# Kernel tuning notes

Measured on AMD Instinct MI355X. Metric: run time of the kernel, lower is better.

The kernel has to match this reference:

```python
import jax, jax.numpy as jnp
import numpy as np

D_MODEL, N_HEAD, D_HEAD = 192, 12, 16
S, B, RLEN = 1024, 4, 2048
LN_EPS = 1e-12


def _xavier(key, shape):
    fan_in, fan_out = shape[0], int(np.prod(shape[1:]))
    limit = float(np.sqrt(6.0 / (fan_in + fan_out)))
    return jax.random.uniform(key, shape, jnp.float32, -limit, limit)


def setup_inputs() -> dict:
    key = jax.random.key(0)
    ks = jax.random.split(key, 12)
    inp = {
        "x": jax.random.normal(ks[0], (S, B, D_MODEL), jnp.float32),
        "r": jax.random.normal(ks[1], (RLEN, B, D_MODEL), jnp.float32),
        "mask0": jnp.zeros((S, S, B, 1), jnp.float32),
        "Wq": _xavier(ks[2], (D_MODEL, N_HEAD, D_HEAD)),
        "Wk": _xavier(ks[3], (D_MODEL, N_HEAD, D_HEAD)),
        "Wv": _xavier(ks[4], (D_MODEL, N_HEAD, D_HEAD)),
        "Wo": _xavier(ks[5], (D_MODEL, N_HEAD, D_HEAD)),
        "Wr": _xavier(ks[6], (D_MODEL, N_HEAD, D_HEAD)),
        "r_w_bias": _xavier(ks[7], (N_HEAD, D_HEAD)),
        "r_r_bias": _xavier(ks[8], (N_HEAD, D_HEAD)),
        "ln_w": jnp.ones((D_MODEL,), jnp.float32),
        "ln_b": jnp.zeros((D_MODEL,), jnp.float32),
    }
    return inp


def _rel_shift_bnij(x, klen):
    # x: [b, n, i, j] with j = rlen; XLNet relative shift, keep first klen cols
    b, n, i, j = x.shape
    x = x.reshape(b, n, j, i)[:, :, 1:, :].reshape(b, n, i, j - 1)
    return x[:, :, :, :klen]


def reference(x, r, mask0, Wq, Wk, Wv, Wo, Wr, r_w_bias, r_r_bias, ln_w, ln_b):
    mask0 = jnp.zeros_like(mask0)  # Model.forward zeroes the mask
    q_head = jnp.einsum("ibh,hnd->ibnd", x, Wq)
    k_head = jnp.einsum("ibh,hnd->ibnd", x, Wk)
    v_head = jnp.einsum("ibh,hnd->ibnd", x, Wv)
    k_head_r = jnp.einsum("ibh,hnd->ibnd", r, Wr)

    # content-based score
    ac = jnp.einsum("ibnd,jbnd->bnij", q_head + r_w_bias, k_head)
    # position-based score with relative shift
    bd = jnp.einsum("ibnd,jbnd->bnij", q_head + r_r_bias, k_head_r)
    bd = _rel_shift_bnij(bd, ac.shape[3])
    # seg_mat is None -> segment term ef = 0

    scale = 1.0 / np.sqrt(D_HEAD)
    attn_score = (ac + bd) * scale
    attn_score = attn_score - 1e30 * jnp.einsum("ijbn->bnij", mask0)
    attn_prob = jax.nn.softmax(attn_score, axis=3)

    attn_vec = jnp.einsum("bnij,jbnd->ibnd", attn_prob, v_head)
    attn_out = jnp.einsum("ibnd,hnd->ibh", attn_vec, Wo)

    out = attn_out + x  # residual
    mean = jnp.mean(out, axis=-1, keepdims=True)
    var = jnp.mean(jnp.square(out - mean), axis=-1, keepdims=True)
    out = (out - mean) * jax.lax.rsqrt(var + LN_EPS) * ln_w + ln_b
    return out
```

## Files before the change

kernel.cpp:

```cpp
#include <hip/hip_runtime.h>
#include <hip/hip_bf16.h>

#define SQ   1024
#define BB   4
#define DM   192
#define NH   12
#define DH   16
#define RL   2048
#define BN   (BB*NH)

typedef __attribute__((ext_vector_type(8))) short  short8;
typedef __attribute__((ext_vector_type(4))) float  f32x4;
typedef __attribute__((ext_vector_type(2))) unsigned u32x2;
typedef __attribute__((ext_vector_type(4))) unsigned u32x4;

__device__ __forceinline__ short f2bf(float f) {
    unsigned u = __float_as_uint(f);
    u += 0x7fff + ((u >> 16) & 1);
    return (short)(u >> 16);
}
__device__ __forceinline__ unsigned pkbf(float lo, float hi) {
    union { __hip_bfloat162 h; unsigned u; } cv;
    cv.h = __float22bfloat162_rn(make_float2(lo, hi));
    return cv.u;
}
#define P32SWAP(a, b) asm volatile("v_permlane32_swap_b32 %0, %1" : "+v"(a), "+v"(b))
#define P16SWAP(a, b) asm volatile("v_permlane16_swap_b32 %0, %1" : "+v"(a), "+v"(b))

__global__ __launch_bounds__(256) void k_prep(
    const float* __restrict__ x, const float* __restrict__ r,
    const float* __restrict__ Wq, const float* __restrict__ Wk,
    const float* __restrict__ Wv, const float* __restrict__ Wr,
    const float* __restrict__ Wo,
    unsigned short* __restrict__ xb, unsigned short* __restrict__ rb,
    unsigned short* __restrict__ WTq, unsigned short* __restrict__ WTk,
    unsigned short* __restrict__ WTv, unsigned short* __restrict__ WTr,
    unsigned short* __restrict__ Wob)
{
    int idx = blockIdx.x * 256 + threadIdx.x;
    if (idx < 786432) { xb[idx] = (unsigned short)f2bf(x[idx]); return; }
    idx -= 786432;
    if (idx < 1572864) { rb[idx] = (unsigned short)f2bf(r[idx]); return; }
    idx -= 1572864;
    if (idx < 36864) { int nd = idx / 192, h = idx % 192;
                       WTq[idx] = (unsigned short)f2bf(Wq[h*192 + nd]); return; }
    idx -= 36864;
    if (idx < 36864) { int nd = idx / 192, h = idx % 192;
                       WTk[idx] = (unsigned short)f2bf(Wk[h*192 + nd]); return; }
    idx -= 36864;
    if (idx < 36864) { int nd = idx / 192, h = idx % 192;
                       WTv[idx] = (unsigned short)f2bf(Wv[h*192 + nd]); return; }
    idx -= 36864;
    if (idx < 36864) { int nd = idx / 192, h = idx % 192;
                       WTr[idx] = (unsigned short)f2bf(Wr[h*192 + nd]); return; }
    idx -= 36864;
    if (idx < 36864) { Wob[idx] = (unsigned short)f2bf(Wo[idx]); return; }
}

__global__ __launch_bounds__(256) void k_gemm_xr(
    const unsigned short* __restrict__ xb, const unsigned short* __restrict__ rbm,
    const unsigned short* __restrict__ WTq, const unsigned short* __restrict__ WTk,
    const unsigned short* __restrict__ WTv, const unsigned short* __restrict__ WTr,
    const float* __restrict__ rwb, const float* __restrict__ rrb,
    unsigned short* __restrict__ qwb, unsigned short* __restrict__ qrb,
    unsigned short* __restrict__ kh, unsigned short* __restrict__ vh,
    unsigned short* __restrict__ kr)
{
    int bid = blockIdx.x;
    int tid = threadIdx.x, w = tid >> 6, lane = tid & 63, g = lane >> 4, mm = lane & 15;
    if (bid < 2304) {
        int rt = bid / 9, ch = bid % 9;
        int wsel = ch / 3, sub = ch % 3;
        int c0 = sub * 64 + w * 16;
        const unsigned short* WT = (wsel == 0) ? WTq : ((wsel == 1) ? WTk : WTv);
        const unsigned short* arow = xb + (size_t)(rt*16 + mm) * 192 + 8*g;
        const unsigned short* brow = WT + (size_t)(c0 + mm) * 192 + 8*g;
        f32x4 acc = {0.f, 0.f, 0.f, 0.f};
        #pragma unroll
        for (int kk = 0; kk < 6; ++kk) {
            short8 a = *(const short8*)(arow + kk*32);
            short8 b = *(const short8*)(brow + kk*32);
            acc = __builtin_amdgcn_mfma_f32_16x16x32_bf16(a, b, acc, 0, 0, 0);
        }
        int col = c0 + mm, n = col >> 4, d = col & 15;
        if (wsel == 0) {
            const float SCL = 0.3606737602222409f;
            float bw = rwb[col], br = rrb[col];
            #pragma unroll
            for (int r = 0; r < 4; ++r) {
                int row = rt*16 + 4*g + r;
                int i = row >> 2, b2 = row & 3;
                size_t o = ((size_t)(b2*NH + n) * SQ + i) * DH + d;
                qwb[o] = (unsigned short)f2bf((acc[r] + bw) * SCL);
                qrb[o] = (unsigned short)f2bf((acc[r] + br) * SCL);
            }
        } else {
            unsigned short* dst = (wsel == 1) ? kh : vh;
            #pragma unroll
            for (int r = 0; r < 4; ++r) {
                int row = rt*16 + 4*g + r;
                int i = row >> 2, b2 = row & 3;
                size_t o = ((size_t)(b2*NH + n) * SQ + i) * DH + d;
                dst[o] = (unsigned short)f2bf(acc[r]);
            }
        }
    } else {
        int bb = bid - 2304;
        int rt = bb / 3, sub = bb % 3;
        int c0 = sub * 64 + w * 16;
        const unsigned short* arow = rbm + (size_t)(rt*16 + mm) * 192 + 8*g;
        const unsigned short* brow = WTr + (size_t)(c0 + mm) * 192 + 8*g;
        f32x4 acc = {0.f, 0.f, 0.f, 0.f};
        #pragma unroll
        for (int kk = 0; kk < 6; ++kk) {
            short8 a = *(const short8*)(arow + kk*32);
            short8 b = *(const short8*)(brow + kk*32);
            acc = __builtin_amdgcn_mfma_f32_16x16x32_bf16(a, b, acc, 0, 0, 0);
        }
        int col = c0 + mm, n = col >> 4, d = col & 15;
        #pragma unroll
        for (int r = 0; r < 4; ++r) {
            int row = rt*16 + 4*g + r;
            int j = row >> 2, b2 = row & 3;
            kr[((size_t)(b2*NH + n) * RL + j) * DH + d] = (unsigned short)f2bf(acc[r]);
        }
    }
}

__global__ __launch_bounds__(256, 3) void k_attn_mfma(
    const unsigned short* __restrict__ qwb, const unsigned short* __restrict__ qrb,
    const unsigned short* __restrict__ kh, const unsigned short* __restrict__ vh,
    const unsigned short* __restrict__ kr, unsigned short* __restrict__ av_b)
{
    __shared__ __align__(16) short kbuf[2][64*16];
    __shared__ __align__(16) short vbuf[2][64*16];
    __shared__ __align__(16) short rbuf[256*16];
    __shared__ __align__(16) float bdls[4][80*20];

    int bid = blockIdx.x;
    int logical = (bid & 7) * 96 + (bid >> 3);
    int bn = logical >> 4;
    int i0b = (logical & 15) * 64;
    int tid = threadIdx.x, w = tid >> 6, lane = tid & 63;
    int g = lane >> 4, mm = lane & 15;
    size_t headK = (size_t)bn * SQ * DH;
    size_t headR = (size_t)bn * RL * DH;

    short8 qwf = {0,0,0,0,0,0,0,0}, qrf = {0,0,0,0,0,0,0,0};
    if (g < 2) {
        int qrow = i0b + 16*w + mm;
        qwf = *(const short8*)((const short*)qwb + headK + (size_t)qrow*DH + 8*g);
        qrf = *(const short8*)((const short*)qrb + headK + (size_t)qrow*DH + 8*g);
    }

    {
        int hh = tid & 1;
        if (tid < 128) {
            int rr2 = tid >> 1;
            *(u32x4*)(&kbuf[0][rr2*16 + hh*8]) =
                *(const u32x4*)(kh + headK + (size_t)rr2*16 + hh*8);
        } else {
            int rr2 = (tid - 128) >> 1;
            *(u32x4*)(&vbuf[0][rr2*16 + hh*8]) =
                *(const u32x4*)(vh + headK + (size_t)rr2*16 + hh*8);
        }
        int rr2 = tid >> 1;
        int m = 960 - i0b + rr2;
        *(u32x4*)(&rbuf[(m & 255)*16 + hh*8]) =
            *(const u32x4*)(kr + headR + (size_t)m*16 + hh*8);
    }
    __syncthreads();

    float Lacc = 0.f;
    f32x4 opv = {0.f,0.f,0.f,0.f};
    float* bw_ = &bdls[w][0];
    const int basew0 = 1008 - i0b - 16*w;
    const f32x4 z = {0.f,0.f,0.f,0.f};

    for (int t = 0; t < 16; ++t) {
        int cur = t & 1;
        u32x4 sa = {0,0,0,0}, sb = {0,0,0,0};
        bool ds = (t < 15);
        if (ds) {
            if (w == 0) {
                const unsigned short* p = kh + headK + (size_t)(64*(t+1) + lane)*16;
                sa = *(const u32x4*)p; sb = *(const u32x4*)(p + 8);
            } else if (w == 1) {
                const unsigned short* p = vh + headK + (size_t)(64*(t+1) + lane)*16;
                sa = *(const u32x4*)p; sb = *(const u32x4*)(p + 8);
            } else if (w == 2) {
                int m = 1088 + 64*t - i0b + lane;
                const unsigned short* p = kr + headR + (size_t)m*16;
                sa = *(const u32x4*)p; sb = *(const u32x4*)(p + 8);
            }
        }

        int mb = basew0 + 64*t;
        #pragma unroll
        for (int tau = 0; tau < 5; ++tau) {
            int mr = (mb + 16*tau + mm) & 255;
            short8 ra = *(const short8*)(rbuf + mr*16 + 8*(g & 1));
            f32x4 bd = __builtin_amdgcn_mfma_f32_16x16x32_bf16(ra, qrf, z, 0, 0, 0);
            #pragma unroll
            for (int r = 0; r < 4; ++r)
                bw_[(16*tau + 4*g + r)*20 + mm] = bd[r];
        }

        unsigned pk[8]; float Lc = 0.f;
        #pragma unroll
        for (int tp = 0; tp < 4; ++tp) {
            short8 ka = *(const short8*)(&kbuf[cur][(16*tp + mm)*16 + 8*(g & 1)]);
            f32x4 ac = __builtin_amdgcn_mfma_f32_16x16x32_bf16(ka, qwf, z, 0, 0, 0);
            float p0 = __builtin_amdgcn_exp2f(ac[0] + bw_[(16*tp + 4*g + 0 + 16 - mm)*20 + mm]);
            float p1 = __builtin_amdgcn_exp2f(ac[1] + bw_[(16*tp + 4*g + 1 + 16 - mm)*20 + mm]);
            float p2 = __builtin_amdgcn_exp2f(ac[2] + bw_[(16*tp + 4*g + 2 + 16 - mm)*20 + mm]);
            float p3 = __builtin_amdgcn_exp2f(ac[3] + bw_[(16*tp + 4*g + 3 + 16 - mm)*20 + mm]);
            Lc += (p0 + p1) + (p2 + p3);
            pk[2*tp]     = pkbf(p0, p1);
            pk[2*tp + 1] = pkbf(p2, p3);
        }
        Lacc += Lc;

        P32SWAP(pk[0], pk[2]); P16SWAP(pk[0], pk[2]);
        P32SWAP(pk[1], pk[3]); P16SWAP(pk[1], pk[3]);
        P32SWAP(pk[4], pk[6]); P16SWAP(pk[4], pk[6]);
        P32SWAP(pk[5], pk[7]); P16SWAP(pk[5], pk[7]);

        unsigned vb0 = (unsigned)(size_t)(&vbuf[cur][0])
                     + ((unsigned)mm << 3) + ((unsigned)g << 8);
        {
            u32x2 t0, t1;
            asm volatile("ds_read_b64_tr_b16 %0, %2 offset:0\n\t"
                         "ds_read_b64_tr_b16 %1, %2 offset:128\n\t"
                         "s_waitcnt lgkmcnt(0)"
                         : "=&v"(t0), "=&v"(t1) : "v"(vb0));
            __builtin_amdgcn_sched_barrier(0);
            union { unsigned u[4]; short8 s; } va, pb;
            va.u[0]=t0[0]; va.u[1]=t0[1]; va.u[2]=t1[0]; va.u[3]=t1[1];
            pb.u[0]=pk[0]; pb.u[1]=pk[1]; pb.u[2]=pk[2]; pb.u[3]=pk[3];
            opv = __builtin_amdgcn_mfma_f32_16x16x32_bf16(va.s, pb.s, opv, 0, 0, 0);
        }
        {
            u32x2 t0, t1;
            asm volatile("ds_read_b64_tr_b16 %0, %2 offset:0\n\t"
                         "ds_read_b64_tr_b16 %1, %2 offset:128\n\t"
                         "s_waitcnt lgkmcnt(0)"
                         : "=&v"(t0), "=&v"(t1) : "v"(vb0 + 1024));
            __builtin_amdgcn_sched_barrier(0);
            union { unsigned u[4]; short8 s; } va, pb;
            va.u[0]=t0[0]; va.u[1]=t0[1]; va.u[2]=t1[0]; va.u[3]=t1[1];
            pb.u[0]=pk[4]; pb.u[1]=pk[5]; pb.u[2]=pk[6]; pb.u[3]=pk[7];
            opv = __builtin_amdgcn_mfma_f32_16x16x32_bf16(va.s, pb.s, opv, 0, 0, 0);
        }

        if (ds) {
            if (w == 0) {
                *(u32x4*)(&kbuf[cur^1][lane*16])     = sa;
                *(u32x4*)(&kbuf[cur^1][lane*16 + 8]) = sb;
            } else if (w == 1) {
                *(u32x4*)(&vbuf[cur^1][lane*16])     = sa;
                *(u32x4*)(&vbuf[cur^1][lane*16 + 8]) = sb;
            } else if (w == 2) {
                int ms = (1088 + 64*t - i0b + lane) & 255;
                *(u32x4*)(&rbuf[ms*16])     = sa;
                *(u32x4*)(&rbuf[ms*16 + 8]) = sb;
            }
        }
        __syncthreads();
    }

    Lacc += __shfl_xor(Lacc, 16);
    Lacc += __shfl_xor(Lacc, 32);
    float inv = 1.0f / Lacc;
    int b2 = bn / NH, nn = bn % NH;
    int i = i0b + 16*w + mm;
    unsigned o0 = pkbf(opv[0]*inv, opv[1]*inv);
    unsigned o1 = pkbf(opv[2]*inv, opv[3]*inv);
    u32x2 ov = {o0, o1};
    *(u32x2*)(av_b + ((size_t)i*4 + b2)*192 + nn*16 + 4*g) = ov;
}

__global__ __launch_bounds__(256) void k_out_ln(
    const unsigned short* __restrict__ avb, const unsigned short* __restrict__ Wob,
    const float* __restrict__ x,
    const float* __restrict__ lnw, const float* __restrict__ lnb,
    float* __restrict__ out)
{
    __shared__ __align__(16) float os[16][196];
    int tid = threadIdx.x, w = tid >> 6, lane = tid & 63, g = lane >> 4, mm = lane & 15;
    int rt = blockIdx.x;
    const unsigned short* arow = avb + (size_t)(rt*16 + mm)*192 + 8*g;
    short8 a[6];
    #pragma unroll
    for (int kk = 0; kk < 6; ++kk) a[kk] = *(const short8*)(arow + kk*32);
    #pragma unroll
    for (int s = 0; s < 3; ++s) {
        int c0 = w*48 + s*16;
        const unsigned short* brow = Wob + (size_t)(c0 + mm)*192 + 8*g;
        f32x4 acc = {0.f,0.f,0.f,0.f};
        #pragma unroll
        for (int kk = 0; kk < 6; ++kk) {
            short8 b = *(const short8*)(brow + kk*32);
            acc = __builtin_amdgcn_mfma_f32_16x16x32_bf16(a[kk], b, acc, 0, 0, 0);
        }
        int col = c0 + mm;
        #pragma unroll
        for (int r = 0; r < 4; ++r) {
            int rl = 4*g + r;
            os[rl][col] = acc[r] + x[(size_t)(rt*16 + rl)*192 + col];
        }
    }
    __syncthreads();
    int row = tid >> 4, seg = tid & 15;
    const float* ors = &os[row][0] + seg*12;
    f32x4 v0 = *(const f32x4*)(ors);
    f32x4 v1 = *(const f32x4*)(ors + 4);
    f32x4 v2 = *(const f32x4*)(ors + 8);
    float s1 = ((v0[0]+v0[1])+(v0[2]+v0[3])) + ((v1[0]+v1[1])+(v1[2]+v1[3]))
             + ((v2[0]+v2[1])+(v2[2]+v2[3]));
    float q1 = ((v0[0]*v0[0]+v0[1]*v0[1])+(v0[2]*v0[2]+v0[3]*v0[3]))
             + ((v1[0]*v1[0]+v1[1]*v1[1])+(v1[2]*v1[2]+v1[3]*v1[3]))
             + ((v2[0]*v2[0]+v2[1]*v2[1])+(v2[2]*v2[2]+v2[3]*v2[3]));
    #pragma unroll
    for (int off = 1; off < 16; off <<= 1) {
        s1 += __shfl_xor(s1, off);
        q1 += __shfl_xor(q1, off);
    }
    float mean = s1 * (1.0f / 192.0f);
    float var  = q1 * (1.0f / 192.0f) - mean * mean;
    float rstd = rsqrtf(var + 1e-12f);
    int c0 = seg * 12;
    size_t ro = (size_t)(rt*16 + row) * 192;
    #pragma unroll
    for (int c = 0; c < 12; ++c) {
        float v = (c < 4) ? v0[c] : ((c < 8) ? v1[c-4] : v2[c-8]);
        out[ro + c0 + c] = (v - mean) * rstd * lnw[c0 + c] + lnb[c0 + c];
    }
}

extern "C" void kernel_launch(void* const* d_in, const int* in_sizes, int n_in,
                              void* d_out, int out_size, void* d_ws, size_t ws_size,
                              hipStream_t stream) {
    const float* x   = (const float*)d_in[0];
    const float* r   = (const float*)d_in[1];
    const float* Wq  = (const float*)d_in[3];
    const float* Wk  = (const float*)d_in[4];
    const float* Wv  = (const float*)d_in[5];
    const float* Wo  = (const float*)d_in[6];
    const float* Wr  = (const float*)d_in[7];
    const float* rwb = (const float*)d_in[8];
    const float* rrb = (const float*)d_in[9];
    const float* lnw = (const float*)d_in[10];
    const float* lnb = (const float*)d_in[11];
    float* out = (float*)d_out;

    char* ws = (char*)d_ws;
    unsigned short* qwb = (unsigned short*)(ws + 0);
    unsigned short* qrb = (unsigned short*)(ws + 1572864);
    unsigned short* kh  = (unsigned short*)(ws + 3145728);
    unsigned short* vh  = (unsigned short*)(ws + 4718592);
    unsigned short* kr  = (unsigned short*)(ws + 6291456);
    unsigned short* avb = (unsigned short*)(ws + 9437184);
    unsigned short* xb  = (unsigned short*)(ws + 11010048);
    unsigned short* rb  = (unsigned short*)(ws + 12582912);
    unsigned short* WTq = (unsigned short*)(ws + 15728640);
    unsigned short* WTk = (unsigned short*)(ws + 15802368);
    unsigned short* WTv = (unsigned short*)(ws + 15876096);
    unsigned short* WTr = (unsigned short*)(ws + 15949824);
    unsigned short* Wob = (unsigned short*)(ws + 16023552);

    k_prep<<<dim3(9936), dim3(256), 0, stream>>>(x, r, Wq, Wk, Wv, Wr, Wo,
                                                 xb, rb, WTq, WTk, WTv, WTr, Wob);
    k_gemm_xr<<<dim3(3840), dim3(256), 0, stream>>>(xb, rb, WTq, WTk, WTv, WTr,
                                                    rwb, rrb, qwb, qrb, kh, vh, kr);
    k_attn_mfma<<<dim3(768), dim3(256), 0, stream>>>(qwb, qrb, kh, vh, kr, avb);
    k_out_ln<<<dim3(256), dim3(256), 0, stream>>>(avb, Wob, x, lnw, lnb, out);
}
```

Baseline: 70.31 us.

## Load K and R fragments directly into registers and double row tiles in projection GEMM

The attention kernel stops staging K and relative-position K through shared memory. Each wave now loads its MFMA operand fragments straight from global memory into registers, prefetching the next tile, and only V remains in LDS. The bd scratch layout is transposed so that MFMA results are written as one vector store. Separately, the projection GEMM computes two 16-row tiles per block so each B fragment is reused, which halves the grid. The cost is more register pressure and redundant global loads across waves, which may hurt occupancy.

```diff
diff --git a/kernel.cpp b/kernel.cpp
--- a/kernel.cpp
+++ b/kernel.cpp
@@ -23,6 +23,9 @@
     union { __hip_bfloat162 h; unsigned u; } cv;
     cv.h = __float22bfloat162_rn(make_float2(lo, hi));
     return cv.u;
+}
+__device__ __forceinline__ short8 as_s8(u32x4 v) {
+    union { u32x4 u; short8 s; } c; c.u = v; return c.s;
 }
 #define P32SWAP(a, b) asm volatile("v_permlane32_swap_b32 %0, %1" : "+v"(a), "+v"(b))
 #define P16SWAP(a, b) asm volatile("v_permlane16_swap_b32 %0, %1" : "+v"(a), "+v"(b))
@@ -68,19 +71,22 @@
 {
     int bid = blockIdx.x;
     int tid = threadIdx.x, w = tid >> 6, lane = tid & 63, g = lane >> 4, mm = lane & 15;
-    if (bid < 2304) {
-        int rt = bid / 9, ch = bid % 9;
+    if (bid < 1152) {
+        int rt2 = bid / 9, ch = bid % 9;
         int wsel = ch / 3, sub = ch % 3;
         int c0 = sub * 64 + w * 16;
         const unsigned short* WT = (wsel == 0) ? WTq : ((wsel == 1) ? WTk : WTv);
-        const unsigned short* arow = xb + (size_t)(rt*16 + mm) * 192 + 8*g;
+        const unsigned short* arow0 = xb + (size_t)(rt2*32 + mm) * 192 + 8*g;
+        const unsigned short* arow1 = arow0 + 16*192;
         const unsigned short* brow = WT + (size_t)(c0 + mm) * 192 + 8*g;
-        f32x4 acc = {0.f, 0.f, 0.f, 0.f};
+        f32x4 acc0 = {0.f,0.f,0.f,0.f}, acc1 = {0.f,0.f,0.f,0.f};
         #pragma unroll
         for (int kk = 0; kk < 6; ++kk) {
-            short8 a = *(const short8*)(arow + kk*32);
-            short8 b = *(const short8*)(brow + kk*32);
-            acc = __builtin_amdgcn_mfma_f32_16x16x32_bf16(a, b, acc, 0, 0, 0);
+            short8 b  = *(const short8*)(brow  + kk*32);
+            short8 a0 = *(const short8*)(arow0 + kk*32);
+            short8 a1 = *(const short8*)(arow1 + kk*32);
+            acc0 = __builtin_amdgcn_mfma_f32_16x16x32_bf16(a0, b, acc0, 0, 0, 0);
+            acc1 = __builtin_amdgcn_mfma_f32_16x16x32_bf16(a1, b, acc1, 0, 0, 0);
         }
         int col = c0 + mm, n = col >> 4, d = col & 15;
         if (wsel == 0) {
@@ -88,41 +94,54 @@
             float bw = rwb[col], br = rrb[col];
             #pragma unroll
             for (int r = 0; r < 4; ++r) {
-                int row = rt*16 + 4*g + r;
+                int row = rt2*32 + 4*g + r;
                 int i = row >> 2, b2 = row & 3;
                 size_t o = ((size_t)(b2*NH + n) * SQ + i) * DH + d;
-                qwb[o] = (unsigned short)f2bf((acc[r] + bw) * SCL);
-                qrb[o] = (unsigned short)f2bf((acc[r] + br) * SCL);
+                qwb[o] = (unsigned short)f2bf((acc0[r] + bw) * SCL);
+                qrb[o] = (unsigned short)f2bf((acc0[r] + br) * SCL);
+                int row1 = row + 16;
+                int i1 = row1 >> 2, b21 = row1 & 3;
+                size_t o1 = ((size_t)(b21*NH + n) * SQ + i1) * DH + d;
+                qwb[o1] = (unsigned short)f2bf((acc1[r] + bw) * SCL);
+                qrb[o1] = (unsigned short)f2bf((acc1[r] + br) * SCL);
             }
         } else {
             unsigned short* dst = (wsel == 1) ? kh : vh;
             #pragma unroll
             for (int r = 0; r < 4; ++r) {
-                int row = rt*16 + 4*g + r;
+                int row = rt2*32 + 4*g + r;
                 int i = row >> 2, b2 = row & 3;
-                size_t o = ((size_t)(b2*NH + n) * SQ + i) * DH + d;
-                dst[o] = (unsigned short)f2bf(acc[r]);
+                dst[((size_t)(b2*NH + n) * SQ + i) * DH + d] = (unsigned short)f2bf(acc0[r]);
+                int row1 = row + 16;
+                int i1 = row1 >> 2, b21 = row1 & 3;
+                dst[((size_t)(b21*NH + n) * SQ + i1) * DH + d] = (unsigned short)f2bf(acc1[r]);
             }
         }
     } else {
-        int bb = bid - 2304;
-        int rt = bb / 3, sub = bb % 3;
+        int bb = bid - 1152;
+        int rt2 = bb / 3, sub = bb % 3;
         int c0 = sub * 64 + w * 16;
-        const unsigned short* arow = rbm + (size_t)(rt*16 + mm) * 192 + 8*g;
+        const unsigned short* arow0 = rbm + (size_t)(rt2*32 + mm) * 192 + 8*g;
+        const unsigned short* arow1 = arow0 + 16*192;
         const unsigned short* brow = WTr + (size_t)(c0 + mm) * 192 + 8*g;
-        f32x4 acc = {0.f, 0.f, 0.f, 0.f};
+        f32x4 acc0 = {0.f,0.f,0.f,0.f}, acc1 = {0.f,0.f,0.f,0.f};
         #pragma unroll
         for (int kk = 0; kk < 6; ++kk) {
-            short8 a = *(const short8*)(arow + kk*32);
-            short8 b = *(const short8*)(brow + kk*32);
-            acc = __builtin_amdgcn_mfma_f32_16x16x32_bf16(a, b, acc, 0, 0, 0);
+            short8 b  = *(const short8*)(brow  + kk*32);
+            short8 a0 = *(const short8*)(arow0 + kk*32);
+            short8 a1 = *(const short8*)(arow1 + kk*32);
+            acc0 = __builtin_amdgcn_mfma_f32_16x16x32_bf16(a0, b, acc0, 0, 0, 0);
+            acc1 = __builtin_amdgcn_mfma_f32_16x16x32_bf16(a1, b, acc1, 0, 0, 0);
         }
         int col = c0 + mm, n = col >> 4, d = col & 15;
         #pragma unroll
         for (int r = 0; r < 4; ++r) {
-            int row = rt*16 + 4*g + r;
+            int row = rt2*32 + 4*g + r;
             int j = row >> 2, b2 = row & 3;
-            kr[((size_t)(b2*NH + n) * RL + j) * DH + d] = (unsigned short)f2bf(acc[r]);
+            kr[((size_t)(b2*NH + n) * RL + j) * DH + d] = (unsigned short)f2bf(acc0[r]);
+            int row1 = row + 16;
+            int j1 = row1 >> 2, b21 = row1 & 3;
+            kr[((size_t)(b21*NH + n) * RL + j1) * DH + d] = (unsigned short)f2bf(acc1[r]);
         }
     }
 }
@@ -132,10 +151,8 @@
     const unsigned short* __restrict__ kh, const unsigned short* __restrict__ vh,
     const unsigned short* __restrict__ kr, unsigned short* __restrict__ av_b)
 {
-    __shared__ __align__(16) short kbuf[2][64*16];
     __shared__ __align__(16) short vbuf[2][64*16];
-    __shared__ __align__(16) short rbuf[256*16];
-    __shared__ __align__(16) float bdls[4][80*20];
+    __shared__ __align__(16) float bdls[4][16*84];
 
     int bid = blockIdx.x;
     int logical = (bid & 7) * 96 + (bid >> 3);
@@ -145,6 +162,7 @@
     int g = lane >> 4, mm = lane & 15;
     size_t headK = (size_t)bn * SQ * DH;
     size_t headR = (size_t)bn * RL * DH;
+    int koff = 8 * (g & 1);
 
     short8 qwf = {0,0,0,0,0,0,0,0}, qrf = {0,0,0,0,0,0,0,0};
     if (g < 2) {
@@ -153,68 +171,58 @@
         qrf = *(const short8*)((const short*)qrb + headK + (size_t)qrow*DH + 8*g);
     }
 
-    {
-        int hh = tid & 1;
-        if (tid < 128) {
-            int rr2 = tid >> 1;
-            *(u32x4*)(&kbuf[0][rr2*16 + hh*8]) =
-                *(const u32x4*)(kh + headK + (size_t)rr2*16 + hh*8);
-        } else {
-            int rr2 = (tid - 128) >> 1;
-            *(u32x4*)(&vbuf[0][rr2*16 + hh*8]) =
-                *(const u32x4*)(vh + headK + (size_t)rr2*16 + hh*8);
-        }
-        int rr2 = tid >> 1;
-        int m = 960 - i0b + rr2;
-        *(u32x4*)(&rbuf[(m & 255)*16 + hh*8]) =
-            *(const u32x4*)(kr + headR + (size_t)m*16 + hh*8);
-    }
+    if (tid < 128) {
+        int rr2 = tid >> 1, hh = tid & 1;
+        *(u32x4*)(&vbuf[0][rr2*16 + hh*8]) =
+            *(const u32x4*)(vh + headK + (size_t)rr2*16 + hh*8);
+    }
+    const int basew0 = 1008 - i0b - 16*w;
+    u32x4 ka[4], krg[5], kan[4], krn[5];
+    #pragma unroll
+    for (int tp = 0; tp < 4; ++tp)
+        ka[tp] = *(const u32x4*)(kh + headK + (size_t)(16*tp + mm)*16 + koff);
+    #pragma unroll
+    for (int tau = 0; tau < 5; ++tau)
+        krg[tau] = *(const u32x4*)(kr + headR + (size_t)(basew0 + 16*tau + mm)*16 + koff);
     __syncthreads();
 
     float Lacc = 0.f;
     f32x4 opv = {0.f,0.f,0.f,0.f};
     float* bw_ = &bdls[w][0];
-    const int basew0 = 1008 - i0b - 16*w;
     const f32x4 z = {0.f,0.f,0.f,0.f};
 
     for (int t = 0; t < 16; ++t) {
         int cur = t & 1;
-        u32x4 sa = {0,0,0,0}, sb = {0,0,0,0};
+        u32x4 sva = {0,0,0,0}, svb = {0,0,0,0};
         bool ds = (t < 15);
         if (ds) {
-            if (w == 0) {
-                const unsigned short* p = kh + headK + (size_t)(64*(t+1) + lane)*16;
-                sa = *(const u32x4*)p; sb = *(const u32x4*)(p + 8);
-            } else if (w == 1) {
+            #pragma unroll
+            for (int tp = 0; tp < 4; ++tp)
+                kan[tp] = *(const u32x4*)(kh + headK + (size_t)(64*(t+1) + 16*tp + mm)*16 + koff);
+            #pragma unroll
+            for (int tau = 0; tau < 5; ++tau)
+                krn[tau] = *(const u32x4*)(kr + headR + (size_t)(basew0 + 64*(t+1) + 16*tau + mm)*16 + koff);
+            if (w == 1) {
                 const unsigned short* p = vh + headK + (size_t)(64*(t+1) + lane)*16;
-                sa = *(const u32x4*)p; sb = *(const u32x4*)(p + 8);
-            } else if (w == 2) {
-                int m = 1088 + 64*t - i0b + lane;
-                const unsigned short* p = kr + headR + (size_t)m*16;
-                sa = *(const u32x4*)p; sb = *(const u32x4*)(p + 8);
+                sva = *(const u32x4*)p; svb = *(const u32x4*)(p + 8);
             }
         }
 
-        int mb = basew0 + 64*t;
         #pragma unroll
         for (int tau = 0; tau < 5; ++tau) {
-            int mr = (mb + 16*tau + mm) & 255;
-            short8 ra = *(const short8*)(rbuf + mr*16 + 8*(g & 1));
-            f32x4 bd = __builtin_amdgcn_mfma_f32_16x16x32_bf16(ra, qrf, z, 0, 0, 0);
-            #pragma unroll
-            for (int r = 0; r < 4; ++r)
-                bw_[(16*tau + 4*g + r)*20 + mm] = bd[r];
+            f32x4 bd = __builtin_amdgcn_mfma_f32_16x16x32_bf16(as_s8(krg[tau]), qrf, z, 0, 0, 0);
+            *(f32x4*)(bw_ + mm*84 + 16*tau + 4*g) = bd;
         }
 
         unsigned pk[8]; float Lc = 0.f;
         #pragma unroll
         for (int tp = 0; tp < 4; ++tp) {
-            short8 ka = *(const short8*)(&kbuf[cur][(16*tp + mm)*16 + 8*(g & 1)]);
-            f32x4 ac = __builtin_amdgcn_mfma_f32_16x16x32_bf16(ka, qwf, z, 0, 0, 0);
-            float p0 = __builtin_amdgcn_exp2f(ac[0] + bw_[(16*tp + 4*g + 0 + 16 - mm)*20 + mm]);
-            float p1 = __builtin_amdgcn_exp2f(ac[1] + bw_[(16*tp + 4*g + 1 + 16 - mm)*20 + mm]);
-            float p2 = __builtin_amdgcn_exp2f(ac[2] + bw_[(16*tp + 4*g + 2 + 16 - mm)*20 + mm]);
-            float p3 = __builtin_amdgcn_exp2f(ac[3] + bw_[(16*tp + 4*g + 3 + 16 - mm)*20 + mm]);
+            f32x4 ac = __builtin_amdgcn_mfma_f32_16x16x32_bf16(as_s8(ka[tp]), qwf, z, 0, 0, 0);
+            int cb = mm*84 + 16*tp + 4*g + 16 - mm;
+            float p0 = __builtin_amdgcn_exp2f(ac[0] + bw_[cb + 0]);
+            float p1 = __builtin_amdgcn_exp2f(ac[1] + bw_[cb + 1]);
+            float p2 = __builtin_amdgcn_exp2f(ac[2] + bw_[cb + 2]);
+            float p3 = __builtin_amdgcn_exp2f(ac[3] + bw_[cb + 3]);
             Lc += (p0 + p1) + (p2 + p3);
             pk[2*tp]     = pkbf(p0, p1);
             pk[2*tp + 1] = pkbf(p2, p3);
@@ -254,19 +262,18 @@
         }
 
         if (ds) {
-            if (w == 0) {
-                *(u32x4*)(&kbuf[cur^1][lane*16])     = sa;
-                *(u32x4*)(&kbuf[cur^1][lane*16 + 8]) = sb;
-            } else if (w == 1) {
-                *(u32x4*)(&vbuf[cur^1][lane*16])     = sa;
-                *(u32x4*)(&vbuf[cur^1][lane*16 + 8]) = sb;
-            } else if (w == 2) {
-                int ms = (1088 + 64*t - i0b + lane) & 255;
-                *(u32x4*)(&rbuf[ms*16])     = sa;
-                *(u32x4*)(&rbuf[ms*16 + 8]) = sb;
+            if (w == 1) {
+                *(u32x4*)(&vbuf[cur^1][lane*16])     = sva;
+                *(u32x4*)(&vbuf[cur^1][lane*16 + 8]) = svb;
             }
         }
         __syncthreads();
+        if (ds) {
+            #pragma unroll
+            for (int tp = 0; tp < 4; ++tp) ka[tp] = kan[tp];
+            #pragma unroll
+            for (int tau = 0; tau < 5; ++tau) krg[tau] = krn[tau];
+        }
     }
 
     Lacc += __shfl_xor(Lacc, 16);
@@ -371,7 +378,7 @@
 
     k_prep<<<dim3(9936), dim3(256), 0, stream>>>(x, r, Wq, Wk, Wv, Wr, Wo,
                                                  xb, rb, WTq, WTk, WTv, WTr, Wob);
-    k_gemm_xr<<<dim3(3840), dim3(256), 0, stream>>>(xb, rb, WTq, WTk, WTv, WTr,
+    k_gemm_xr<<<dim3(1920), dim3(256), 0, stream>>>(xb, rb, WTq, WTk, WTv, WTr,
                                                     rwb, rrb, qwb, qrb, kh, vh, kr);
     k_attn_mfma<<<dim3(768), dim3(256), 0, stream>>>(qwb, qrb, kh, vh, kr, avb);
     k_out_ln<<<dim3(256), dim3(256), 0, stream>>>(avb, Wob, x, lnw, lnb, out);
```

Result: faster. 64.85 us (-7.8%).
